# Performance work log

Hardware: AMD Instinct MI355X
Metric: run time of the kernel (lower is better)

## Reference

```python
import jax, jax.numpy as jnp
import numpy as np

TEMPERATURE = 0.1
NORM_EPS = 1e-12   # F.normalize default eps
LOSS_EPS = 1e-6

def _l2norm_c(x):
    # L2-normalize along channel dim (axis=1), matching F.normalize(dim=1)
    n = jnp.sqrt(jnp.sum(x * x, axis=1, keepdims=True))
    return x / jnp.maximum(n, NORM_EPS)

def setup_inputs() -> dict:
    key = jax.random.key(0)
    k1, k2, k3 = jax.random.split(key, 3)
    N, C, H, W = 8, 64, 64, 64
    rgb_map = jax.random.normal(k1, (N, C, H, W), dtype=jnp.float32)
    ir_map = jax.random.normal(k2, (N, C, H, W), dtype=jnp.float32)
    targets = jax.random.randint(k3, (N,), 0, 2)  # unused by the forward math
    return {"rgb_map": rgb_map, "ir_map": ir_map, "targets": targets}

def reference(rgb_map, ir_map, targets):
    N, C, H, W = rgb_map.shape
    rgb = _l2norm_c(rgb_map).reshape(N, C, H * W)   # [N, C, P]
    ir = _l2norm_c(ir_map).reshape(N, C, H * W)     # [N, C, P]
    # [N, P, P] similarity, then temperature exp
    logit = jnp.exp(jnp.einsum('ncp,ncq->npq', rgb, ir) / TEMPERATURE)
    pos = jnp.trace(logit, axis1=1, axis2=2)        # diagonal (positive) sum per sample
    tot = jnp.sum(logit, axis=(-1, -2))             # full row/col sum per sample
    loss = -jnp.log(pos / (tot + LOSS_EPS)).mean()
    return loss
```

## Files before the change

kernel.cpp:

```cpp
#include <hip/hip_runtime.h>

#define N_ 8
#define C_ 64
#define P_ 4096

typedef float f32x4 __attribute__((ext_vector_type(4)));
typedef short bf16x8 __attribute__((ext_vector_type(8)));

__device__ __forceinline__ unsigned short f2bf(float f) {
  unsigned int u = __builtin_bit_cast(unsigned int, f);
  u = (u + 0x7fffu + ((u >> 16) & 1u)) >> 16;
  return (unsigned short)u;
}

__device__ __forceinline__ float exp2appr(float x) {
  const int i = (int)__builtin_fmaf(x, 8388608.0f, 1064992209.0f);
  return __builtin_bit_cast(float, i);
}

__global__ void __launch_bounds__(256) norm_transpose(
    const float* __restrict__ rgb, const float* __restrict__ ir,
    unsigned short* __restrict__ rgbnT, unsigned short* __restrict__ irnT) {
  const int idx = blockIdx.x * 256 + threadIdx.x;
  const int n = idx >> 12;
  const int p = idx & (P_ - 1);
  const float* src = (blockIdx.y == 0) ? rgb : ir;
  unsigned short* dst = (blockIdx.y == 0) ? rgbnT : irnT;
  const float SC = 14.4269504088896340736f;
  const float* col = src + (size_t)n * C_ * P_ + p;
  float v[C_];
  float ss = 0.f;
#pragma unroll
  for (int c = 0; c < C_; ++c) {
    v[c] = col[(size_t)c * P_];
    ss += v[c] * v[c];
  }
  float inv = 1.0f / fmaxf(sqrtf(ss), 1e-12f);
  if (blockIdx.y == 0) inv *= SC;
  const int gx = (blockIdx.y == 0) ? 0 : (p & 7);
  unsigned short* o = dst + ((size_t)n * P_ + p) * C_;
#pragma unroll
  for (int g = 0; g < 8; ++g) {
    bf16x8 pack;
#pragma unroll
    for (int j = 0; j < 8; ++j) pack[j] = (short)f2bf(v[g * 8 + j] * inv);
    *reinterpret_cast<bf16x8*>(o + (g ^ gx) * 8) = pack;
  }
}

__device__ __forceinline__ void stage_tile(const unsigned short* src,
                                           unsigned short* dst, int tid,
                                           int wid) {
#pragma unroll
  for (int r = 0; r < 2; ++r) {
    __builtin_amdgcn_global_load_lds(
        (const __attribute__((address_space(1))) void*)(src +
                                                        (size_t)(r * 256 + tid) * 8),
        (__attribute__((address_space(3))) void*)(dst + (r * 256 + wid * 64) * 8),
        16, 0, 0);
  }
}

__global__ void __launch_bounds__(256) gemm_exp_reduce(
    const unsigned short* __restrict__ aT, const unsigned short* __restrict__ bT,
    float* __restrict__ partials) {
  const int lin = blockIdx.x;
  const int n = lin & 7;
  const int local = lin >> 3;
  const int pc = local & 15;
  const int qc = local >> 4;
  const int tid = threadIdx.x;
  const int lane = tid & 63;
  const int wid = tid >> 6;
  const int pbase = pc * 256 + wid * 64;
  const int q0 = qc * 512;
  const unsigned short* A = aT + (size_t)n * P_ * C_;
  const unsigned short* B = bT + (size_t)n * P_ * C_;
  const int r16 = lane & 15;
  const int kofs = (lane >> 4) * 8;

  __shared__ __align__(16) unsigned short bs0[64 * 64];
  __shared__ __align__(16) unsigned short bs1[64 * 64];
  __shared__ __align__(16) unsigned short bs2[64 * 64];
  __shared__ __align__(16) unsigned short bs3[64 * 64];

  bf16x8 af[2][4];
#pragma unroll
  for (int ks = 0; ks < 2; ++ks)
#pragma unroll
    for (int mi = 0; mi < 4; ++mi)
      af[ks][mi] = *reinterpret_cast<const bf16x8*>(
          A + (size_t)(pbase + mi * 16 + r16) * C_ + ks * 32 + kofs);

  stage_tile(B + (size_t)(q0 + 0 * 64) * C_, bs0, tid, wid);
  stage_tile(B + (size_t)(q0 + 1 * 64) * C_, bs1, tid, wid);
  stage_tile(B + (size_t)(q0 + 2 * 64) * C_, bs2, tid, wid);

  unsigned short *pcur = bs0, *pnx1 = bs1, *pnx2 = bs2, *pnx3 = bs3;

  const f32x4 zc = (f32x4)(0.f);
  float t0 = 0.f, t1 = 0.f, t2 = 0.f, t3 = 0.f, pos = 0.f;
  const int col = lane & 15;
  const int rowb = (lane >> 4) * 4;

#pragma unroll 1
  for (int t = 0; t < 8; ++t) {
    asm volatile("s_waitcnt vmcnt(4)" ::: "memory");
    __builtin_amdgcn_sched_barrier(0);
    __builtin_amdgcn_s_barrier();

    int s = t + 3;
    if (s >= 8) s -= 8;
    stage_tile(B + (size_t)(q0 + s * 64) * C_, pnx3, tid, wid);

    const unsigned short* bp = pcur;
    bf16x8 bf_[2][4];
#pragma unroll
    for (int ks = 0; ks < 2; ++ks)
#pragma unroll
      for (int ni = 0; ni < 4; ++ni) {
        const int row = ni * 16 + r16;
        const int seg = ks * 4 + (lane >> 4);
        bf_[ks][ni] = *reinterpret_cast<const bf16x8*>(
            bp + row * 64 + ((seg ^ (lane & 7)) * 8));
      }

    f32x4 acc[4][4];
    __builtin_amdgcn_s_setprio(1);
#pragma unroll
    for (int mi = 0; mi < 4; ++mi)
#pragma unroll
      for (int ni = 0; ni < 4; ++ni)
        acc[mi][ni] = __builtin_amdgcn_mfma_f32_16x16x32_bf16(
            af[0][mi], bf_[0][ni], zc, 0, 0, 0);
#pragma unroll
    for (int mi = 0; mi < 4; ++mi)
#pragma unroll
      for (int ni = 0; ni < 4; ++ni)
        acc[mi][ni] = __builtin_amdgcn_mfma_f32_16x16x32_bf16(
            af[1][mi], bf_[1][ni], acc[mi][ni], 0, 0, 0);
    __builtin_amdgcn_s_setprio(0);

#pragma unroll
    for (int mi = 0; mi < 4; ++mi)
#pragma unroll
      for (int ni = 0; ni < 4; ++ni) {
        const f32x4 v = acc[mi][ni];
        t0 += exp2appr(v[0]);
        t1 += exp2appr(v[1]);
        t2 += exp2appr(v[2]);
        t3 += exp2appr(v[3]);
      }
    const int qb = q0 + t * 64;
    if (pbase == qb) {
#pragma unroll
      for (int mi = 0; mi < 4; ++mi)
#pragma unroll
        for (int r = 0; r < 4; ++r)
          if (rowb + r == col) pos += exp2appr(acc[mi][mi][r]);
    }

    unsigned short* tmp = pcur;
    pcur = pnx1;
    pnx1 = pnx2;
    pnx2 = pnx3;
    pnx3 = tmp;
  }

  float tot = (t0 + t1) + (t2 + t3);
#pragma unroll
  for (int off = 32; off > 0; off >>= 1) {
    tot += __shfl_down(tot, off);
    pos += __shfl_down(pos, off);
  }
  __shared__ float sb[8];
  if (lane == 0) { sb[wid * 2] = pos; sb[wid * 2 + 1] = tot; }
  __syncthreads();
  if (tid == 0) {
    const float pp = sb[0] + sb[2] + sb[4] + sb[6];
    const float tt = sb[1] + sb[3] + sb[5] + sb[7];
    const int bid = n * 128 + pc * 8 + qc;
    partials[bid * 2] = pp;
    partials[bid * 2 + 1] = tt;
  }
}

__global__ void __launch_bounds__(1024) finalize(
    const float* __restrict__ partials, float* __restrict__ out) {
  const int tid = threadIdx.x;
  const int lane = tid & 63, wid = tid >> 6;
  __shared__ float sp[16], st[16], sl[8];
  const int n = tid >> 7;
  const int i = tid & 127;
  float p = partials[(n * 128 + i) * 2];
  float t = partials[(n * 128 + i) * 2 + 1];
#pragma unroll
  for (int off = 32; off > 0; off >>= 1) {
    p += __shfl_down(p, off);
    t += __shfl_down(t, off);
  }
  if (lane == 0) { sp[wid] = p; st[wid] = t; }
  __syncthreads();
  if (tid < 8) {
    const float pp = sp[2 * tid] + sp[2 * tid + 1];
    const float tt = st[2 * tid] + st[2 * tid + 1];
    sl[tid] = -logf(pp / (tt + 1e-6f));
  }
  __syncthreads();
  if (tid == 0) {
    float loss = 0.f;
#pragma unroll
    for (int k = 0; k < 8; ++k) loss += sl[k];
    out[0] = loss * (1.0f / N_);
  }
}

extern "C" void kernel_launch(void* const* d_in, const int* in_sizes, int n_in,
                              void* d_out, int out_size, void* d_ws, size_t ws_size,
                              hipStream_t stream) {
  const float* rgb = (const float*)d_in[0];
  const float* ir = (const float*)d_in[1];
  float* out = (float*)d_out;

  unsigned short* rgbnT = (unsigned short*)d_ws;
  unsigned short* irnT = rgbnT + (size_t)N_ * P_ * C_;
  float* partials = (float*)(irnT + (size_t)N_ * P_ * C_);

  dim3 g1(N_ * P_ / 256, 2);
  norm_transpose<<<g1, 256, 0, stream>>>(rgb, ir, rgbnT, irnT);

  gemm_exp_reduce<<<1024, 256, 0, stream>>>(rgbnT, irnT, partials);

  finalize<<<1, 1024, 0, stream>>>(partials, out);
}
```

Before: 41.91 us.

## Split channel norm across two thread halves and vectorize exp accumulation with packed f32x2

The normalize/transpose kernel now assigns two threads per pixel, each handling 32 channels, and combines their partial sums of squares through shared memory. This doubles the thread count and halves per-thread register use, giving more memory-level parallelism on the strided loads. In the GEMM epilogue, the approximate exp2 accumulation is rewritten on two-wide float vectors with eight independent accumulator chains, so the compiler can emit packed FMA/add instructions and shorten dependency chains. The cost is an added block barrier in the norm kernel and more accumulator registers in the GEMM.

New measurement: 39.28 us. -6.3%, faster.

```diff
diff --git a/kernel.cpp b/kernel.cpp
--- a/kernel.cpp
+++ b/kernel.cpp
@@ -5,6 +5,7 @@
 #define P_ 4096
 
 typedef float f32x4 __attribute__((ext_vector_type(4)));
+typedef float f32x2 __attribute__((ext_vector_type(2)));
 typedef short bf16x8 __attribute__((ext_vector_type(8)));
 
 __device__ __forceinline__ unsigned short f2bf(float f) {
@@ -21,30 +22,38 @@
 __global__ void __launch_bounds__(256) norm_transpose(
     const float* __restrict__ rgb, const float* __restrict__ ir,
     unsigned short* __restrict__ rgbnT, unsigned short* __restrict__ irnT) {
-  const int idx = blockIdx.x * 256 + threadIdx.x;
-  const int n = idx >> 12;
-  const int p = idx & (P_ - 1);
+  const int tid = threadIdx.x;
+  const int half = tid >> 7;
+  const int pl = tid & 127;
+  const int gp = blockIdx.x * 128 + pl;
+  const int n = gp >> 12;
+  const int p = gp & (P_ - 1);
   const float* src = (blockIdx.y == 0) ? rgb : ir;
   unsigned short* dst = (blockIdx.y == 0) ? rgbnT : irnT;
   const float SC = 14.4269504088896340736f;
-  const float* col = src + (size_t)n * C_ * P_ + p;
-  float v[C_];
+  const float* col = src + (size_t)n * C_ * P_ + (size_t)(half * 32) * P_ + p;
+  float v[32];
   float ss = 0.f;
 #pragma unroll
-  for (int c = 0; c < C_; ++c) {
+  for (int c = 0; c < 32; ++c) {
     v[c] = col[(size_t)c * P_];
     ss += v[c] * v[c];
   }
-  float inv = 1.0f / fmaxf(sqrtf(ss), 1e-12f);
+  __shared__ float ssq[2][128];
+  ssq[half][pl] = ss;
+  __syncthreads();
+  const float tot = ssq[0][pl] + ssq[1][pl];
+  float inv = 1.0f / fmaxf(sqrtf(tot), 1e-12f);
   if (blockIdx.y == 0) inv *= SC;
   const int gx = (blockIdx.y == 0) ? 0 : (p & 7);
-  unsigned short* o = dst + ((size_t)n * P_ + p) * C_;
-#pragma unroll
-  for (int g = 0; g < 8; ++g) {
+  unsigned short* o = dst + (size_t)gp * C_;
+#pragma unroll
+  for (int gi = 0; gi < 4; ++gi) {
     bf16x8 pack;
 #pragma unroll
-    for (int j = 0; j < 8; ++j) pack[j] = (short)f2bf(v[g * 8 + j] * inv);
-    *reinterpret_cast<bf16x8*>(o + (g ^ gx) * 8) = pack;
+    for (int j = 0; j < 8; ++j) pack[j] = (short)f2bf(v[gi * 8 + j] * inv);
+    const int gg = half * 4 + gi;
+    *reinterpret_cast<bf16x8*>(o + (gg ^ gx) * 8) = pack;
   }
 }
 
@@ -99,7 +108,10 @@
   unsigned short *pcur = bs0, *pnx1 = bs1, *pnx2 = bs2, *pnx3 = bs3;
 
   const f32x4 zc = (f32x4)(0.f);
-  float t0 = 0.f, t1 = 0.f, t2 = 0.f, t3 = 0.f, pos = 0.f;
+  f32x2 ch2[8];
+#pragma unroll
+  for (int k = 0; k < 8; ++k) ch2[k] = (f32x2)(0.f);
+  float pos = 0.f;
   const int col = lane & 15;
   const int rowb = (lane >> 4) * 4;
 
@@ -145,11 +157,20 @@
     for (int mi = 0; mi < 4; ++mi)
 #pragma unroll
       for (int ni = 0; ni < 4; ++ni) {
+        const int base = ((mi * 4 + ni) & 3) * 2;
         const f32x4 v = acc[mi][ni];
-        t0 += exp2appr(v[0]);
-        t1 += exp2appr(v[1]);
-        t2 += exp2appr(v[2]);
-        t3 += exp2appr(v[3]);
+        f32x2 a0, a1;
+        a0[0] = v[0]; a0[1] = v[1];
+        a1[0] = v[2]; a1[1] = v[3];
+        const f32x2 f0 = a0 * 8388608.0f + (f32x2)(1064992209.0f);
+        const f32x2 f1 = a1 * 8388608.0f + (f32x2)(1064992209.0f);
+        f32x2 e0, e1;
+        e0[0] = __builtin_bit_cast(float, (int)f0[0]);
+        e0[1] = __builtin_bit_cast(float, (int)f0[1]);
+        e1[0] = __builtin_bit_cast(float, (int)f1[0]);
+        e1[1] = __builtin_bit_cast(float, (int)f1[1]);
+        ch2[base] += e0;
+        ch2[base + 1] += e1;
       }
     const int qb = q0 + t * 64;
     if (pbase == qb) {
@@ -167,7 +188,9 @@
     pnx3 = tmp;
   }
 
-  float tot = (t0 + t1) + (t2 + t3);
+  f32x2 sum2 = ((ch2[0] + ch2[1]) + (ch2[2] + ch2[3])) +
+               ((ch2[4] + ch2[5]) + (ch2[6] + ch2[7]));
+  float tot = sum2[0] + sum2[1];
 #pragma unroll
   for (int off = 32; off > 0; off >>= 1) {
     tot += __shfl_down(tot, off);
@@ -226,7 +249,7 @@
   unsigned short* irnT = rgbnT + (size_t)N_ * P_ * C_;
   float* partials = (float*)(irnT + (size_t)N_ * P_ * C_);
 
-  dim3 g1(N_ * P_ / 256, 2);
+  dim3 g1(N_ * P_ / 128, 2);
   norm_transpose<<<g1, 256, 0, stream>>>(rgb, ir, rgbnT, irnT);
 
   gemm_exp_reduce<<<1024, 256, 0, stream>>>(rgbnT, irnT, partials);
```
